# Kernel tuning notes

Hardware: AMD Instinct MI355X
Metric: run time of the kernel (lower is better)

Reference implementation:

```python
import jax, jax.numpy as jnp
import numpy as np

N = 50000          # nodes
E = 800000         # edges (before self-loops)
IN = 128           # in_dim
HID = 128          # hidden_dim
HEADS = 4
G = 256            # graphs in batch
EPS = 1e-5         # batchnorm eps
NEG_SLOPE = 0.2    # GATConv leaky_relu slope


def _gat_layer(x, src, dst, W, a_src, a_dst, bias, H, C, concat):
    """PyG-style GATConv (self-loops already appended to src/dst)."""
    n = x.shape[0]
    h = (x @ W).reshape(n, H, C)                       # [N,H,C]
    s_src = (h * a_src).sum(-1)                        # [N,H]
    s_dst = (h * a_dst).sum(-1)                        # [N,H]
    e = jax.nn.leaky_relu(s_src[src] + s_dst[dst], NEG_SLOPE)   # [E',H]
    m = jax.ops.segment_max(e, dst, num_segments=n)    # segment-wise softmax
    ex = jnp.exp(e - m[dst])
    den = jax.ops.segment_sum(ex, dst, num_segments=n)
    alpha = ex / den[dst]                              # [E',H]
    out = jax.ops.segment_sum(alpha[..., None] * h[src], dst, num_segments=n)  # [N,H,C]
    out = out.reshape(n, H * C) if concat else out.mean(axis=1)
    return out + bias


def _bn(x, gamma, beta):
    # PyG BatchNorm over nodes (training-mode batch statistics)
    mu = x.mean(axis=0)
    var = x.var(axis=0)
    return gamma * (x - mu) * jax.lax.rsqrt(var + EPS) + beta


def setup_inputs() -> dict:
    key = jax.random.key(0)
    ks = jax.random.split(key, 32)
    d = {}
    d["x"] = jax.random.normal(ks[0], (N, IN), dtype=jnp.float32)
    d["edge_index"] = jax.random.randint(ks[1], (2, E), 0, N, dtype=jnp.int64)
    d["batch_idx"] = jnp.sort(jax.random.randint(ks[2], (N,), 0, G, dtype=jnp.int64))
    dims = [(IN, HEADS, HID, True), (HID * HEADS, HEADS, HID, True), (HID * HEADS, 1, HID, False)]
    for i, (din, H, C, concat) in enumerate(dims):
        d[f"W{i}"] = jax.random.normal(ks[3 + 4 * i], (din, H * C), dtype=jnp.float32) * 0.05
        d[f"att_src{i}"] = jax.random.normal(ks[4 + 4 * i], (H, C), dtype=jnp.float32) * 0.05
        d[f"att_dst{i}"] = jax.random.normal(ks[5 + 4 * i], (H, C), dtype=jnp.float32) * 0.05
        out_w = H * C if concat else C
        d[f"bias{i}"] = jnp.zeros((out_w,), dtype=jnp.float32)
        d[f"gamma{i}"] = jnp.ones((out_w,), dtype=jnp.float32)
        d[f"beta{i}"] = jnp.zeros((out_w,), dtype=jnp.float32)
    return d


def reference(x, edge_index, batch_idx,
              W0, att_src0, att_dst0, bias0, gamma0, beta0,
              W1, att_src1, att_dst1, bias1, gamma1, beta1,
              W2, att_src2, att_dst2, bias2, gamma2, beta2):
    n = x.shape[0]
    loops = jnp.arange(n, dtype=edge_index.dtype)
    src = jnp.concatenate([edge_index[0], loops])
    dst = jnp.concatenate([edge_index[1], loops])
    layers = [
        (W0, att_src0, att_dst0, bias0, gamma0, beta0, HEADS, HID, True),
        (W1, att_src1, att_dst1, bias1, gamma1, beta1, HEADS, HID, True),
        (W2, att_src2, att_dst2, bias2, gamma2, beta2, 1, HID, False),
    ]
    h = x
    for (W, a_s, a_d, b, g, bt, H, C, concat) in layers:
        h = _gat_layer(h, src, dst, W, a_s, a_d, b, H, C, concat)
        h = jax.nn.elu(_bn(h, g, bt))
        # dropout: identity in eval mode
    # global_mean_pool over batch_idx
    sums = jax.ops.segment_sum(h, batch_idx, num_segments=G)
    cnt = jax.ops.segment_sum(jnp.ones((n,), dtype=h.dtype), batch_idx, num_segments=G)
    return sums / jnp.maximum(cnt, 1.0)[:, None]
```

## Files before the change

### kernel.cpp

```cpp
#include <hip/hip_runtime.h>
#include <math.h>
#include <stdint.h>

#define N_NODES 50000
#define NPAD    50048
#define N_EDGES 800000
#define EP      (N_EDGES + N_NODES)
#define G_GRAPHS 256
#define BN_EPS   1e-5f
#define NEG_SLOPE 0.2f

typedef float f32x4 __attribute__((ext_vector_type(4)));
typedef _Float16 h16x8 __attribute__((ext_vector_type(8)));

static __device__ __forceinline__ float lrelu(float x) {
    return x > 0.f ? x : NEG_SLOPE * x;
}

static __device__ __forceinline__ void gld_lds16(const void* g, void* l) {
    __builtin_amdgcn_global_load_lds((const __attribute__((address_space(1))) void*)g,
                                     (__attribute__((address_space(3))) void*)l, 16, 0, 0);
}

static __device__ __forceinline__ float2 h2f2(unsigned u) {
    union { unsigned u; _Float16 h[2]; } c;
    c.u = u;
    return make_float2((float)c.h[0], (float)c.h[1]);
}

__global__ void k_hist(const int* __restrict__ ei, int* __restrict__ deg) {
    int stride = gridDim.x * blockDim.x;
    for (int e = blockIdx.x * blockDim.x + threadIdx.x; e < EP; e += stride) {
        int d = (e < N_EDGES) ? ei[N_EDGES + e] : (e - N_EDGES);
        atomicAdd(&deg[d], 1);
    }
}

__global__ void k_scan1(const int* __restrict__ deg, int* __restrict__ row_start,
                        int* __restrict__ totals) {
    __shared__ int buf[1024];
    int t = threadIdx.x;
    int i = blockIdx.x * 1024 + t;
    int v = (i < N_NODES) ? deg[i] : 0;
    buf[t] = v;
    __syncthreads();
    for (int off = 1; off < 1024; off <<= 1) {
        int add = (t >= off) ? buf[t - off] : 0;
        __syncthreads();
        buf[t] += add;
        __syncthreads();
    }
    if (i < N_NODES) row_start[i] = buf[t] - v;
    if (t == 1023) totals[blockIdx.x] = buf[t];
}

__global__ void k_scan2(int* __restrict__ totals, int nb) {
    if (threadIdx.x == 0 && blockIdx.x == 0) {
        int run = 0;
        for (int i = 0; i < nb; ++i) { int v = totals[i]; totals[i] = run; run += v; }
    }
}

__global__ void k_scan3(int* __restrict__ row_start, const int* __restrict__ totals) {
    int i = blockIdx.x * blockDim.x + threadIdx.x;
    if (i < N_NODES) row_start[i] += totals[i >> 10];
    if (i == 0) row_start[N_NODES] = EP;
}

__global__ void k_scatter(const int* __restrict__ ei, const int* __restrict__ row_start,
                          int* __restrict__ cursor, int* __restrict__ csr_src) {
    int stride = gridDim.x * blockDim.x;
    for (int e = blockIdx.x * blockDim.x + threadIdx.x; e < EP; e += stride) {
        int s, d;
        if (e < N_EDGES) { s = ei[e]; d = ei[N_EDGES + e]; }
        else             { s = d = e - N_EDGES; }
        int pos = row_start[d] + atomicAdd(&cursor[d], 1);
        csr_src[pos] = s;
    }
}

__global__ void k_cvtW(const float* __restrict__ W, _Float16* __restrict__ bthi,
                       int Nc, int nsh, int KS) {
    int i = blockIdx.x * 256 + threadIdx.x;
    if (i >= (KS << 5) * Nc) return;
    int k = i >> nsh;
    int n = i & (Nc - 1);
    int c = n >> 7, col = n & 127;
    int ks = k >> 5, kq = (k >> 3) & 3, j = k & 7;
    size_t idx = ((size_t)(c * KS + ks) << 12) + (kq << 10) + (col << 3) + j;
    bthi[idx] = (_Float16)W[i];
}

__global__ void k_bnprep(const float* __restrict__ bnsum, const float* __restrict__ bnsq,
                         const float* __restrict__ gamma, const float* __restrict__ beta,
                         float* __restrict__ scale, float* __restrict__ shift, int W) {
    int f = blockIdx.x * 256 + threadIdx.x;
    if (f >= W) return;
    const float invN = 1.f / (float)N_NODES;
    float mean = bnsum[f] * invN;
    float var  = bnsq[f] * invN - mean * mean;
    float sc = gamma[f] * rsqrtf(var + BN_EPS);
    scale[f] = sc;
    shift[f] = beta[f] - mean * sc;
}

__global__ void k_prepA0(const float* __restrict__ x, _Float16* __restrict__ Aswz,
                         int K, int s8, int KS) {
    int i = blockIdx.x * 256 + threadIdx.x;
    if (i >= NPAD * (K >> 3)) return;
    int r  = i >> s8;
    int c8 = i & ((K >> 3) - 1);
    int k  = c8 << 3;
    union { _Float16 h[8]; uint4 u; } pk;
    if (r < N_NODES) {
        float4 a0 = *(const float4*)&x[(size_t)r * K + k];
        float4 a1 = *(const float4*)&x[(size_t)r * K + k + 4];
        pk.h[0]=(_Float16)a0.x; pk.h[1]=(_Float16)a0.y; pk.h[2]=(_Float16)a0.z; pk.h[3]=(_Float16)a0.w;
        pk.h[4]=(_Float16)a1.x; pk.h[5]=(_Float16)a1.y; pk.h[6]=(_Float16)a1.z; pk.h[7]=(_Float16)a1.w;
    } else {
        pk.u.x = pk.u.y = pk.u.z = pk.u.w = 0u;
    }
    int rb = r >> 7, row = r & 127;
    int ks = k >> 5, kq = (k >> 3) & 3;
    size_t idx = ((size_t)(rb * KS + ks) << 12) + (kq << 10) + (row << 3);
    *(uint4*)&Aswz[idx] = pk.u;
}

__global__ void k_prepA1(const _Float16* __restrict__ act, const float* __restrict__ scale,
                         const float* __restrict__ shift, _Float16* __restrict__ Aswz,
                         int K, int s8, int KS) {
    int i = blockIdx.x * 256 + threadIdx.x;
    if (i >= NPAD * (K >> 3)) return;
    int r  = i >> s8;
    int c8 = i & ((K >> 3) - 1);
    int k  = c8 << 3;
    union { _Float16 h[8]; uint4 u; } pk;
    if (r < N_NODES) {
        uint4 v = *(const uint4*)&act[(size_t)r * K + k];
        float4 sc0 = *(const float4*)&scale[k];
        float4 sc1 = *(const float4*)&scale[k + 4];
        float4 sh0 = *(const float4*)&shift[k];
        float4 sh1 = *(const float4*)&shift[k + 4];
        float2 p0 = h2f2(v.x), p1 = h2f2(v.y), p2 = h2f2(v.z), p3 = h2f2(v.w);
        float y;
        y = fmaf(p0.x, sc0.x, sh0.x); pk.h[0] = (_Float16)(y > 0.f ? y : expm1f(y));
        y = fmaf(p0.y, sc0.y, sh0.y); pk.h[1] = (_Float16)(y > 0.f ? y : expm1f(y));
        y = fmaf(p1.x, sc0.z, sh0.z); pk.h[2] = (_Float16)(y > 0.f ? y : expm1f(y));
        y = fmaf(p1.y, sc0.w, sh0.w); pk.h[3] = (_Float16)(y > 0.f ? y : expm1f(y));
        y = fmaf(p2.x, sc1.x, sh1.x); pk.h[4] = (_Float16)(y > 0.f ? y : expm1f(y));
        y = fmaf(p2.y, sc1.y, sh1.y); pk.h[5] = (_Float16)(y > 0.f ? y : expm1f(y));
        y = fmaf(p3.x, sc1.z, sh1.z); pk.h[6] = (_Float16)(y > 0.f ? y : expm1f(y));
        y = fmaf(p3.y, sc1.w, sh1.w); pk.h[7] = (_Float16)(y > 0.f ? y : expm1f(y));
    } else {
        pk.u.x = pk.u.y = pk.u.z = pk.u.w = 0u;
    }
    int rb = r >> 7, row = r & 127;
    int ks = k >> 5, kq = (k >> 3) & 3;
    size_t idx = ((size_t)(rb * KS + ks) << 12) + (kq << 10) + (row << 3);
    *(uint4*)&Aswz[idx] = pk.u;
}

__launch_bounds__(256)
__global__ void k_gemm_f16(const _Float16* __restrict__ Aswz, const _Float16* __restrict__ bthi,
                           _Float16* __restrict__ C2,
                           float* __restrict__ sSg, float* __restrict__ sDg,
                           const float* __restrict__ asr, const float* __restrict__ adr,
                           int M, int K, int Nc) {
    __shared__ _Float16 Ah[4096], Bh[4096];
    __shared__ float rS[128], rD[128];
    const int t    = threadIdx.x;
    const int lane = t & 63, wv = t >> 6;
    const int wr = wv >> 1, wc = wv & 1;
    const int lr = lane & 15, kq = lane >> 4;
    const int r0 = blockIdx.x * 128, c0 = blockIdx.y * 128;
    const int KS = K >> 5;
    const int H = Nc >> 7;
    const int head = blockIdx.y;

    const size_t achunk0 = (size_t)blockIdx.x * KS * 4096;
    const size_t bchunk0 = (size_t)blockIdx.y * KS * 4096;

    f32x4 acc[4][4];
    #pragma unroll
    for (int m = 0; m < 4; ++m)
        #pragma unroll
        for (int n = 0; n < 4; ++n) {
            acc[m][n][0] = 0.f; acc[m][n][1] = 0.f;
            acc[m][n][2] = 0.f; acc[m][n][3] = 0.f;
        }

    for (int ks = 0; ks < KS; ++ks) {
        __syncthreads();
        const _Float16* as  = Aswz + achunk0 + ((size_t)ks << 12);
        const _Float16* bhs = bthi + bchunk0 + ((size_t)ks << 12);
        #pragma unroll
        for (int p = 0; p < 2; ++p) {
            int ge = p * 2048 + wv * 512 + lane * 8;
            int le = p * 2048 + wv * 512;
            gld_lds16(as  + ge, &Ah[le]);
            gld_lds16(bhs + ge, &Bh[le]);
        }
        __syncthreads();

        h16x8 af[4], bfh[4];
        #pragma unroll
        for (int m = 0; m < 4; ++m) {
            int row = wr * 64 + m * 16 + lr;
            af[m] = *(const h16x8*)&Ah[kq * 1024 + row * 8];
        }
        #pragma unroll
        for (int n = 0; n < 4; ++n) {
            int col = wc * 64 + n * 16 + lr;
            bfh[n] = *(const h16x8*)&Bh[kq * 1024 + col * 8];
        }
        #pragma unroll
        for (int m = 0; m < 4; ++m)
            #pragma unroll
            for (int n = 0; n < 4; ++n)
                acc[m][n] = __builtin_amdgcn_mfma_f32_16x16x32_f16(af[m], bfh[n], acc[m][n], 0, 0, 0);
    }

    float aS[4], aD[4];
    #pragma unroll
    for (int n = 0; n < 4; ++n) {
        int c = c0 + wc * 64 + n * 16 + lr;
        aS[n] = asr[c];
        aD[n] = adr[c];
    }
    __syncthreads();
    if (t < 128) { rS[t] = 0.f; rD[t] = 0.f; }
    __syncthreads();
    #pragma unroll
    for (int m = 0; m < 4; ++m) {
        #pragma unroll
        for (int j = 0; j < 4; ++j) {
            float ps = 0.f, pd = 0.f;
            #pragma unroll
            for (int n = 0; n < 4; ++n) {
                float v = acc[m][n][j];
                ps += v * aS[n];
                pd += v * aD[n];
            }
            #pragma unroll
            for (int off = 1; off < 16; off <<= 1) {
                ps += __shfl_xor(ps, off, 64);
                pd += __shfl_xor(pd, off, 64);
            }
            if (lr == 0) {
                int row = wr * 64 + m * 16 + kq * 4 + j;
                atomicAdd(&rS[row], ps);
                atomicAdd(&rD[row], pd);
            }
        }
    }
    __syncthreads();
    if (t < 128) {
        int r = r0 + t;
        if (r < M) {
            sSg[(size_t)r * H + head] = rS[t];
            sDg[(size_t)r * H + head] = rD[t];
        }
    }

    #pragma unroll
    for (int m = 0; m < 4; ++m) {
        int rowb = r0 + wr * 64 + m * 16 + kq * 4;
        #pragma unroll
        for (int n = 0; n < 4; ++n) {
            int col = c0 + wc * 64 + n * 16 + lr;
            #pragma unroll
            for (int j = 0; j < 4; ++j) {
                int r = rowb + j;
                if (r < M) C2[(size_t)r * Nc + col] = (_Float16)acc[m][n][j];
            }
        }
    }
}

template<int H, int CPT, int CAP>
__launch_bounds__(256)
__global__ void k_attnagg(const _Float16* __restrict__ hb2, const float* __restrict__ s_src,
                          const float* __restrict__ s_dst, const int* __restrict__ row_start,
                          const int* __restrict__ csr, const float* __restrict__ bias,
                          _Float16* __restrict__ out) {
    const int W = H * 128;
    __shared__ float alds[4][CAP * H];
    const int wv = threadIdx.x >> 6;
    const int lane = threadIdx.x & 63;
    const int n = blockIdx.x * 4 + wv;
    if (n >= N_NODES) return;
    const int lo = row_start[n], hi = row_start[n + 1];
    const int deg = hi - lo;

    const int h1 = lane & (H - 1);
    const int eo = lane / H;
    const int EPI = 64 / H;
    float sd1 = s_dst[n * H + h1];
    const int c0 = lane * CPT;
    const int myh = c0 >> 7;
    float* al = &alds[wv][0];

    float acc[CPT];
    #pragma unroll
    for (int j = 0; j < CPT; ++j) acc[j] = 0.f;
    float invv;

    if (deg <= CAP) {
        float mx = -INFINITY;
        for (int q = eo; q < deg; q += EPI) {
            float e = lrelu(s_src[csr[lo + q] * H + h1] + sd1);
            al[q * H + h1] = e;
            mx = fmaxf(mx, e);
        }
        #pragma unroll
        for (int off = H; off < 64; off <<= 1) mx = fmaxf(mx, __shfl_xor(mx, off, 64));
        float sum = 0.f;
        for (int q = eo; q < deg; q += EPI) {
            float ex = expf(al[q * H + h1] - mx);
            al[q * H + h1] = ex;
            sum += ex;
        }
        #pragma unroll
        for (int off = H; off < 64; off <<= 1) sum += __shfl_xor(sum, off, 64);
        invv = __shfl(1.f / sum, myh, 64);
        asm volatile("s_waitcnt lgkmcnt(0)" ::: "memory");
        __builtin_amdgcn_sched_barrier(0);

        for (int q = 0; q < deg; q += 16) {
            int s[16];
            float a[16];
            #pragma unroll
            for (int j = 0; j < 16; ++j) {
                int qq = q + j;
                int qc = qq < deg ? qq : deg - 1;
                s[j] = csr[lo + qc];
                a[j] = (qq < deg) ? al[qc * H + myh] : 0.f;
            }
            if constexpr (CPT == 8) {
                uint4 v[16];
                #pragma unroll
                for (int j = 0; j < 16; ++j) v[j] = *(const uint4*)&hb2[(size_t)s[j] * W + c0];
                #pragma unroll
                for (int j = 0; j < 16; ++j) {
                    float2 x0 = h2f2(v[j].x), x1 = h2f2(v[j].y), x2 = h2f2(v[j].z), x3 = h2f2(v[j].w);
                    acc[0] += a[j]*x0.x; acc[1] += a[j]*x0.y; acc[2] += a[j]*x1.x; acc[3] += a[j]*x1.y;
                    acc[4] += a[j]*x2.x; acc[5] += a[j]*x2.y; acc[6] += a[j]*x3.x; acc[7] += a[j]*x3.y;
                }
            } else {
                unsigned v[16];
                #pragma unroll
                for (int j = 0; j < 16; ++j) v[j] = *(const unsigned*)&hb2[(size_t)s[j] * W + c0];
                #pragma unroll
                for (int j = 0; j < 16; ++j) {
                    float2 x = h2f2(v[j]);
                    acc[0] += a[j]*x.x; acc[1] += a[j]*x.y;
                }
            }
        }
    } else {
        float mx = -INFINITY;
        for (int p = lo + eo; p < hi; p += EPI) {
            float e = lrelu(s_src[csr[p] * H + h1] + sd1);
            mx = fmaxf(mx, e);
        }
        #pragma unroll
        for (int off = H; off < 64; off <<= 1) mx = fmaxf(mx, __shfl_xor(mx, off, 64));
        float sum = 0.f;
        for (int p = lo + eo; p < hi; p += EPI) {
            float e = lrelu(s_src[csr[p] * H + h1] + sd1);
            sum += expf(e - mx);
        }
        #pragma unroll
        for (int off = H; off < 64; off <<= 1) sum += __shfl_xor(sum, off, 64);
        float inv = 1.f / sum;
        float mxv = __shfl(mx, myh, 64);
        invv = __shfl(inv, myh, 64);
        float sdv = __shfl(sd1, myh, 64);
        for (int p = lo; p < hi; ++p) {
            int s0 = csr[p];
            float a0 = expf(lrelu(s_src[s0 * H + myh] + sdv) - mxv);
            if constexpr (CPT == 8) {
                uint4 v0 = *(const uint4*)&hb2[(size_t)s0 * W + c0];
                float2 x0 = h2f2(v0.x), x1 = h2f2(v0.y), x2 = h2f2(v0.z), x3 = h2f2(v0.w);
                acc[0] += a0*x0.x; acc[1] += a0*x0.y; acc[2] += a0*x1.x; acc[3] += a0*x1.y;
                acc[4] += a0*x2.x; acc[5] += a0*x2.y; acc[6] += a0*x3.x; acc[7] += a0*x3.y;
            } else {
                float2 x = h2f2(*(const unsigned*)&hb2[(size_t)s0 * W + c0]);
                acc[0] += a0*x.x; acc[1] += a0*x.y;
            }
        }
    }

    union { _Float16 h[CPT]; uint4 u4; unsigned u1; } pk;
    #pragma unroll
    for (int j = 0; j < CPT; ++j) pk.h[j] = (_Float16)(fmaf(acc[j], invv, bias[c0 + j]));
    if constexpr (CPT == 8)
        *(uint4*)&out[(size_t)n * W + c0] = pk.u4;
    else
        *(unsigned*)&out[(size_t)n * W + c0] = pk.u1;
}

__global__ void k_bnstat2(const _Float16* __restrict__ x, float* __restrict__ bnsum,
                          float* __restrict__ bnsq, int W) {
    const int RPB = 64;
    int t  = threadIdx.x;
    int r0 = blockIdx.x * RPB;
    int r1 = min(r0 + RPB, N_NODES);
    float s0 = 0.f, q0 = 0.f, s1 = 0.f, q1 = 0.f;
    for (int r = r0; r < r1; ++r) {
        float2 v = h2f2(*(const unsigned*)&x[(size_t)r * W + 2 * t]);
        s0 += v.x; q0 += v.x * v.x;
        s1 += v.y; q1 += v.y * v.y;
    }
    atomicAdd(&bnsum[2*t],   s0);
    atomicAdd(&bnsq[2*t],    q0);
    atomicAdd(&bnsum[2*t+1], s1);
    atomicAdd(&bnsq[2*t+1],  q1);
}

__global__ void k_pool(const _Float16* __restrict__ x, const int* __restrict__ batch,
                       const float* __restrict__ scale, const float* __restrict__ shift,
                       float* __restrict__ out) {
    int g = blockIdx.x;
    int f = threadIdx.x;
    int a = 0, b = N_NODES;
    while (a < b) { int m = (a + b) >> 1; if (batch[m] < g) a = m + 1; else b = m; }
    int lo = a;
    b = N_NODES;
    while (a < b) { int m = (a + b) >> 1; if (batch[m] < g + 1) a = m + 1; else b = m; }
    int hi = a;
    float sc = scale[f], sh = shift[f];
    float s = 0.f;
    for (int r = lo; r < hi; ++r) {
        float v = (float)x[(size_t)r * 128 + f];
        float y = fmaf(v, sc, sh);
        s += (y > 0.f) ? y : expm1f(y);
    }
    int cnt = hi - lo;
    out[g * 128 + f] = s / (float)(cnt > 0 ? cnt : 1);
}

extern "C" void kernel_launch(void* const* d_in, const int* in_sizes, int n_in,
                              void* d_out, int out_size, void* d_ws, size_t ws_size,
                              hipStream_t stream) {
    const float* x     = (const float*)d_in[0];
    const int*   ei    = (const int*)d_in[1];
    const int*   batch = (const int*)d_in[2];
    const float* Wm[3]  = {(const float*)d_in[3],  (const float*)d_in[9],  (const float*)d_in[15]};
    const float* asr[3] = {(const float*)d_in[4],  (const float*)d_in[10], (const float*)d_in[16]};
    const float* adr[3] = {(const float*)d_in[5],  (const float*)d_in[11], (const float*)d_in[17]};
    const float* bia[3] = {(const float*)d_in[6],  (const float*)d_in[12], (const float*)d_in[18]};
    const float* gam[3] = {(const float*)d_in[7],  (const float*)d_in[13], (const float*)d_in[19]};
    const float* bet[3] = {(const float*)d_in[8],  (const float*)d_in[14], (const float*)d_in[20]};

    char* w = (char*)d_ws;
    auto alloc = [&](size_t bytes) -> void* {
        void* p = (void*)w;
        w += (bytes + 255) & ~(size_t)255;
        return p;
    };
    _Float16* act2   = (_Float16*)alloc((size_t)N_NODES * 512 * 2);
    _Float16* act128 = (_Float16*)alloc((size_t)N_NODES * 128 * 2);
    _Float16* hb2    = (_Float16*)alloc((size_t)N_NODES * 512 * 2);
    _Float16* Aswz   = (_Float16*)alloc((size_t)NPAD * 512 * 2);
    int* csr_src   = (int*)alloc((size_t)EP * 4);
    int* row_start = (int*)alloc((size_t)(N_NODES + 1) * 4);
    int* deg       = (int*)alloc((size_t)N_NODES * 4);
    int* cursor    = (int*)alloc((size_t)N_NODES * 4);
    float* s_src = (float*)alloc((size_t)N_NODES * 4 * 4);
    float* s_dst = (float*)alloc((size_t)N_NODES * 4 * 4);
    float* bn    = (float*)alloc(1024 * 4);
    float* scl   = (float*)alloc(512 * 4);
    float* shf   = (float*)alloc(512 * 4);
    int* totals  = (int*)alloc(64 * 4);
    _Float16* bthi = (_Float16*)alloc((size_t)512 * 512 * 2);

    hipMemsetAsync(deg, 0, (size_t)N_NODES * 4, stream);
    hipMemsetAsync(cursor, 0, (size_t)N_NODES * 4, stream);
    k_hist<<<512, 256, 0, stream>>>(ei, deg);
    k_scan1<<<(N_NODES + 1023) / 1024, 1024, 0, stream>>>(deg, row_start, totals);
    k_scan2<<<1, 64, 0, stream>>>(totals, (N_NODES + 1023) / 1024);
    k_scan3<<<(N_NODES + 255) / 256, 256, 0, stream>>>(row_start, totals);
    k_scatter<<<512, 256, 0, stream>>>(ei, row_start, cursor, csr_src);

    auto layer = [&](int K, int li, int H, bool first, _Float16* outAct) {
        int Wd = H * 128;
        int nsh = (Wd == 512) ? 9 : 7;
        int KS = K >> 5;
        int s8 = (K == 512) ? 6 : 4;
        int tot = K * Wd;
        k_cvtW<<<(tot + 255) / 256, 256, 0, stream>>>(Wm[li], bthi, Wd, nsh, KS);
        int ptot = NPAD * (K >> 3);
        if (first)
            k_prepA0<<<(ptot + 255) / 256, 256, 0, stream>>>(x, Aswz, K, s8, KS);
        else
            k_prepA1<<<(ptot + 255) / 256, 256, 0, stream>>>(act2, scl, shf, Aswz, K, s8, KS);
        dim3 gg(NPAD / 128, Wd / 128);
        k_gemm_f16<<<gg, 256, 0, stream>>>(Aswz, bthi, hb2, s_src, s_dst,
                                           asr[li], adr[li], N_NODES, K, Wd);
        int nb = (N_NODES + 3) / 4;
        if (H == 4)
            k_attnagg<4, 8, 256><<<nb, 256, 0, stream>>>(hb2, s_src, s_dst, row_start, csr_src,
                                                         bia[li], outAct);
        else
            k_attnagg<1, 2, 256><<<nb, 256, 0, stream>>>(hb2, s_src, s_dst, row_start, csr_src,
                                                         bia[li], outAct);
        hipMemsetAsync(bn, 0, 1024 * 4, stream);
        k_bnstat2<<<(N_NODES + 63) / 64, Wd / 2, 0, stream>>>(outAct, bn, bn + 512, Wd);
        k_bnprep<<<(Wd + 255) / 256, 256, 0, stream>>>(bn, bn + 512, gam[li], bet[li], scl, shf, Wd);
    };

    layer(128, 0, 4, true,  act2);
    layer(512, 1, 4, false, act2);
    layer(512, 2, 1, false, act128);

    k_pool<<<G_GRAPHS, 128, 0, stream>>>(act128, batch, scl, shf, (float*)d_out);
}
```

Baseline: 852.1 us.

## Double-buffer GEMM LDS tiles and make swizzle-prep writes contiguous

The GEMM main loop now double-buffers the A and B tiles in LDS, issuing the next k-slice's global-to-LDS loads before computing on the current one, with explicit vmcnt waits and barriers. This is meant to hide global load latency behind the MFMA work. The weight-conversion and activation-prep kernels are re-indexed so each thread writes one contiguous 16-byte chunk of the swizzled layout, with reads now gathered instead. The cost is doubled LDS per block, which may lower occupancy, and the hand-tuned waitcnt logic is more fragile.

```diff
diff --git a/kernel.cpp b/kernel.cpp
--- a/kernel.cpp
+++ b/kernel.cpp
@@ -80,15 +80,23 @@
 }
 
 __global__ void k_cvtW(const float* __restrict__ W, _Float16* __restrict__ bthi,
-                       int Nc, int nsh, int KS) {
-    int i = blockIdx.x * 256 + threadIdx.x;
-    if (i >= (KS << 5) * Nc) return;
-    int k = i >> nsh;
-    int n = i & (Nc - 1);
-    int c = n >> 7, col = n & 127;
-    int ks = k >> 5, kq = (k >> 3) & 3, j = k & 7;
-    size_t idx = ((size_t)(c * KS + ks) << 12) + (kq << 10) + (col << 3) + j;
-    bthi[idx] = (_Float16)W[i];
+                       int Nc, int lgKS) {
+    int idx8 = blockIdx.x * 256 + threadIdx.x;
+    int KS = 1 << lgKS;
+    int total = ((KS << 5) * Nc) >> 3;
+    if (idx8 >= total) return;
+    int col = idx8 & 127;
+    int kq  = (idx8 >> 7) & 3;
+    int cs  = idx8 >> 9;
+    int ks  = cs & (KS - 1);
+    int c   = cs >> lgKS;
+    int n = (c << 7) + col;
+    int k = (ks << 5) + (kq << 3);
+    union { _Float16 h[8]; uint4 u; } pk;
+    #pragma unroll
+    for (int j = 0; j < 8; ++j)
+        pk.h[j] = (_Float16)W[(size_t)(k + j) * Nc + n];
+    *(uint4*)&bthi[(size_t)idx8 * 8] = pk.u;
 }
 
 __global__ void k_bnprep(const float* __restrict__ bnsum, const float* __restrict__ bnsq,
@@ -105,12 +113,17 @@
 }
 
 __global__ void k_prepA0(const float* __restrict__ x, _Float16* __restrict__ Aswz,
-                         int K, int s8, int KS) {
-    int i = blockIdx.x * 256 + threadIdx.x;
-    if (i >= NPAD * (K >> 3)) return;
-    int r  = i >> s8;
-    int c8 = i & ((K >> 3) - 1);
-    int k  = c8 << 3;
+                         int K, int lgKS) {
+    int idx8 = blockIdx.x * 256 + threadIdx.x;
+    int total = NPAD * (K >> 3);
+    if (idx8 >= total) return;
+    int row = idx8 & 127;
+    int kq  = (idx8 >> 7) & 3;
+    int cs  = idx8 >> 9;
+    int ks  = cs & ((1 << lgKS) - 1);
+    int rb  = cs >> lgKS;
+    int r = (rb << 7) + row;
+    int k = (ks << 5) + (kq << 3);
     union { _Float16 h[8]; uint4 u; } pk;
     if (r < N_NODES) {
         float4 a0 = *(const float4*)&x[(size_t)r * K + k];
@@ -120,20 +133,22 @@
     } else {
         pk.u.x = pk.u.y = pk.u.z = pk.u.w = 0u;
     }
-    int rb = r >> 7, row = r & 127;
-    int ks = k >> 5, kq = (k >> 3) & 3;
-    size_t idx = ((size_t)(rb * KS + ks) << 12) + (kq << 10) + (row << 3);
-    *(uint4*)&Aswz[idx] = pk.u;
+    *(uint4*)&Aswz[(size_t)idx8 * 8] = pk.u;
 }
 
 __global__ void k_prepA1(const _Float16* __restrict__ act, const float* __restrict__ scale,
                          const float* __restrict__ shift, _Float16* __restrict__ Aswz,
-                         int K, int s8, int KS) {
-    int i = blockIdx.x * 256 + threadIdx.x;
-    if (i >= NPAD * (K >> 3)) return;
-    int r  = i >> s8;
-    int c8 = i & ((K >> 3) - 1);
-    int k  = c8 << 3;
+                         int K, int lgKS) {
+    int idx8 = blockIdx.x * 256 + threadIdx.x;
+    int total = NPAD * (K >> 3);
+    if (idx8 >= total) return;
+    int row = idx8 & 127;
+    int kq  = (idx8 >> 7) & 3;
+    int cs  = idx8 >> 9;
+    int ks  = cs & ((1 << lgKS) - 1);
+    int rb  = cs >> lgKS;
+    int r = (rb << 7) + row;
+    int k = (ks << 5) + (kq << 3);
     union { _Float16 h[8]; uint4 u; } pk;
     if (r < N_NODES) {
         uint4 v = *(const uint4*)&act[(size_t)r * K + k];
@@ -154,10 +169,7 @@
     } else {
         pk.u.x = pk.u.y = pk.u.z = pk.u.w = 0u;
     }
-    int rb = r >> 7, row = r & 127;
-    int ks = k >> 5, kq = (k >> 3) & 3;
-    size_t idx = ((size_t)(rb * KS + ks) << 12) + (kq << 10) + (row << 3);
-    *(uint4*)&Aswz[idx] = pk.u;
+    *(uint4*)&Aswz[(size_t)idx8 * 8] = pk.u;
 }
 
 __launch_bounds__(256)
@@ -166,7 +178,7 @@
                            float* __restrict__ sSg, float* __restrict__ sDg,
                            const float* __restrict__ asr, const float* __restrict__ adr,
                            int M, int K, int Nc) {
-    __shared__ _Float16 Ah[4096], Bh[4096];
+    __shared__ _Float16 Ah[2][4096], Bh[2][4096];
     __shared__ float rS[128], rD[128];
     const int t    = threadIdx.x;
     const int lane = t & 63, wv = t >> 6;
@@ -179,6 +191,8 @@
 
     const size_t achunk0 = (size_t)blockIdx.x * KS * 4096;
     const size_t bchunk0 = (size_t)blockIdx.y * KS * 4096;
+    const int ge0 = wv * 512 + lane * 8;
+    const int le0 = wv * 512;
 
     f32x4 acc[4][4];
     #pragma unroll
@@ -189,35 +203,51 @@
             acc[m][n][2] = 0.f; acc[m][n][3] = 0.f;
         }
 
+    {
+        const _Float16* as  = Aswz + achunk0;
+        const _Float16* bhs = bthi + bchunk0;
+        #pragma unroll
+        for (int p = 0; p < 2; ++p) {
+            gld_lds16(as  + p * 2048 + ge0, &Ah[0][p * 2048 + le0]);
+            gld_lds16(bhs + p * 2048 + ge0, &Bh[0][p * 2048 + le0]);
+        }
+    }
+
     for (int ks = 0; ks < KS; ++ks) {
-        __syncthreads();
-        const _Float16* as  = Aswz + achunk0 + ((size_t)ks << 12);
-        const _Float16* bhs = bthi + bchunk0 + ((size_t)ks << 12);
-        #pragma unroll
-        for (int p = 0; p < 2; ++p) {
-            int ge = p * 2048 + wv * 512 + lane * 8;
-            int le = p * 2048 + wv * 512;
-            gld_lds16(as  + ge, &Ah[le]);
-            gld_lds16(bhs + ge, &Bh[le]);
-        }
-        __syncthreads();
+        const int cur = ks & 1;
+        if (ks + 1 < KS) {
+            const _Float16* as  = Aswz + achunk0 + ((size_t)(ks + 1) << 12);
+            const _Float16* bhs = bthi + bchunk0 + ((size_t)(ks + 1) << 12);
+            #pragma unroll
+            for (int p = 0; p < 2; ++p) {
+                gld_lds16(as  + p * 2048 + ge0, &Ah[cur ^ 1][p * 2048 + le0]);
+                gld_lds16(bhs + p * 2048 + ge0, &Bh[cur ^ 1][p * 2048 + le0]);
+            }
+            asm volatile("s_waitcnt vmcnt(4)" ::: "memory");
+        } else {
+            asm volatile("s_waitcnt vmcnt(0)" ::: "memory");
+        }
+        __builtin_amdgcn_s_barrier();
 
         h16x8 af[4], bfh[4];
         #pragma unroll
         for (int m = 0; m < 4; ++m) {
             int row = wr * 64 + m * 16 + lr;
-            af[m] = *(const h16x8*)&Ah[kq * 1024 + row * 8];
+            af[m] = *(const h16x8*)&Ah[cur][kq * 1024 + row * 8];
         }
         #pragma unroll
         for (int n = 0; n < 4; ++n) {
             int col = wc * 64 + n * 16 + lr;
-            bfh[n] = *(const h16x8*)&Bh[kq * 1024 + col * 8];
+            bfh[n] = *(const h16x8*)&Bh[cur][kq * 1024 + col * 8];
         }
         #pragma unroll
         for (int m = 0; m < 4; ++m)
             #pragma unroll
             for (int n = 0; n < 4; ++n)
                 acc[m][n] = __builtin_amdgcn_mfma_f32_16x16x32_f16(af[m], bfh[n], acc[m][n], 0, 0, 0);
+
+        asm volatile("s_waitcnt lgkmcnt(0)" ::: "memory");
+        __builtin_amdgcn_s_barrier();
     }
 
     float aS[4], aD[4];
@@ -485,16 +515,14 @@
 
     auto layer = [&](int K, int li, int H, bool first, _Float16* outAct) {
         int Wd = H * 128;
-        int nsh = (Wd == 512) ? 9 : 7;
-        int KS = K >> 5;
-        int s8 = (K == 512) ? 6 : 4;
-        int tot = K * Wd;
-        k_cvtW<<<(tot + 255) / 256, 256, 0, stream>>>(Wm[li], bthi, Wd, nsh, KS);
+        int lgKS = (K == 512) ? 4 : 2;
+        int tot8 = (K * Wd) >> 3;
+        k_cvtW<<<(tot8 + 255) / 256, 256, 0, stream>>>(Wm[li], bthi, Wd, lgKS);
         int ptot = NPAD * (K >> 3);
         if (first)
-            k_prepA0<<<(ptot + 255) / 256, 256, 0, stream>>>(x, Aswz, K, s8, KS);
+            k_prepA0<<<(ptot + 255) / 256, 256, 0, stream>>>(x, Aswz, K, lgKS);
         else
-            k_prepA1<<<(ptot + 255) / 256, 256, 0, stream>>>(act2, scl, shf, Aswz, K, s8, KS);
+            k_prepA1<<<(ptot + 255) / 256, 256, 0, stream>>>(act2, scl, shf, Aswz, K, lgKS);
         dim3 gg(NPAD / 128, Wd / 128);
         k_gemm_f16<<<gg, 256, 0, stream>>>(Aswz, bthi, hb2, s_src, s_dst,
                                            asr[li], adr[li], N_NODES, K, Wd);
```

After: 876.4 us. +2.9%, slower.
